# Kernel optimization log

Measured on AMD Instinct MI355X. Metric: run time of the kernel, lower is better.

## Reference

```python
import jax, jax.numpy as jnp
import numpy as np

N_SOURCE = 100000
N_TARGET = 4096
DEG = 800                      # edges per target (uniform)
N_EDGES = N_TARGET * DEG       # 3,276,800
SOURCE_DIM = 512
EMBED_DIM = 32
TARGET_DIM = 16


def setup_inputs() -> dict:
    key = jax.random.key(0)
    k1, k2, k3, k4, k5 = jax.random.split(key, 5)
    source_feat = jax.random.normal(k1, (N_SOURCE, SOURCE_DIM), dtype=jnp.float32)
    embed = jax.random.normal(k2, (SOURCE_DIM, EMBED_DIM), dtype=jnp.float32)
    weight = jax.random.normal(k3, (EMBED_DIM, TARGET_DIM), dtype=jnp.float32)
    # edges sorted by target; range_list[i] = [start, end) of target i's edge block
    src = jax.random.randint(k4, (N_EDGES,), 0, N_SOURCE, dtype=jnp.int64)
    tgt = jnp.repeat(jnp.arange(N_TARGET, dtype=jnp.int64), DEG)
    edge_index = jnp.stack([src, tgt], axis=0)
    starts = jnp.arange(N_TARGET, dtype=jnp.int64) * DEG
    range_list = jnp.stack([starts, starts + DEG], axis=1)
    x_norm = jax.random.uniform(k5, (N_SOURCE,), dtype=jnp.float32) + 0.5
    return {"source_feat": source_feat, "embed": embed, "weight": weight,
            "edge_index": edge_index, "range_list": range_list, "x_norm": x_norm}


def reference(source_feat, embed, weight, edge_index, range_list, x_norm):
    # dense embed GEMM + row normalization
    x = jnp.matmul(source_feat, embed)              # [N_SOURCE, EMBED_DIM]
    x = x / x_norm[:, None]
    # hierarchical conv: gather source rows, mean-aggregate per target segment
    tmp = x[edge_index[0]]                           # [N_EDGES, EMBED_DIM]
    agg = jax.ops.segment_sum(tmp, edge_index[1], num_segments=N_TARGET)
    deg = (range_list[:, 1] - range_list[:, 0]).astype(x.dtype)
    out = agg / jnp.maximum(deg, 1.0)[:, None]       # [N_TARGET, EMBED_DIM]
    out = jnp.matmul(out, weight)                    # [N_TARGET, TARGET_DIM]
    return out
```

## Files before the change

### kernel.cpp

```cpp
#include <hip/hip_runtime.h>
#include <hip/hip_bf16.h>

#define N_SOURCE   100000
#define N_TARGET   4096
#define SOURCE_DIM 512
#define EMBED_DIM  32
#define TARGET_DIM 16
#define NTILES     ((N_SOURCE + 15) / 16)

typedef __attribute__((ext_vector_type(8))) short short8;
typedef __attribute__((ext_vector_type(4))) float f32x4;

static __device__ __forceinline__ ushort f2bf(float f) {
    __hip_bfloat16 h = __float2bfloat16(f);
    return *(ushort*)&h;
}

__global__ __launch_bounds__(256)
void k_embed_weight(const float* __restrict__ embed,
                    const float* __restrict__ weight,
                    ushort* __restrict__ Mt) {
    __shared__ float wlds[EMBED_DIM * TARGET_DIM];
    int tid = threadIdx.x;
    for (int i = tid; i < EMBED_DIM * TARGET_DIM; i += 256)
        wlds[i] = weight[i];
    __syncthreads();

    int idx = blockIdx.x * 256 + tid;
    if (idx < SOURCE_DIM * TARGET_DIM) {
        int k = idx >> 4;
        int o = idx & 15;
        float s = 0.f;
        #pragma unroll
        for (int j = 0; j < EMBED_DIM; ++j)
            s += embed[k * EMBED_DIM + j] * wlds[j * TARGET_DIM + o];
        Mt[o * SOURCE_DIM + k] = f2bf(s);
    }
}

__global__ __launch_bounds__(256, 8)
void k_gemm_y(const float*  __restrict__ A,
              const float*  __restrict__ xnorm,
              const ushort* __restrict__ Mt,
              ushort*       __restrict__ y) {
    __shared__ ushort Bl[SOURCE_DIM * TARGET_DIM];
    int tid  = threadIdx.x;
    int wave = tid >> 6;
    int lane = tid & 63;
    int n    = lane & 15;
    int g    = lane >> 4;

    #pragma unroll
    for (int i = 0; i < 4; ++i) {
        int c  = tid + 256 * i;
        int nn = c & 15;
        int kg = c >> 4;
        int kk = kg >> 2;
        int gg = kg & 3;
        *(uint4*)&Bl[c * 8] =
            *(const uint4*)(Mt + nn * SOURCE_DIM + kk * 32 + gg * 8);
    }
    __syncthreads();

    int tile = blockIdx.x * 4 + wave;
    if (tile < NTILES) {
        int row0 = tile * 16;
        const float* Arow = A + (size_t)(row0 + n) * SOURCE_DIM + g * 8;
        const ushort* Bll = Bl + lane * 8;

        f32x4 acc = {0.f, 0.f, 0.f, 0.f};
        #pragma unroll
        for (int kk = 0; kk < 16; ++kk) {
            float4 a0 = *(const float4*)(Arow + kk * 32);
            float4 a1 = *(const float4*)(Arow + kk * 32 + 4);
            short8 bf = *(const short8*)(Bll + kk * 512);
            short8 af;
            af[0] = (short)f2bf(a0.x); af[1] = (short)f2bf(a0.y);
            af[2] = (short)f2bf(a0.z); af[3] = (short)f2bf(a0.w);
            af[4] = (short)f2bf(a1.x); af[5] = (short)f2bf(a1.y);
            af[6] = (short)f2bf(a1.z); af[7] = (short)f2bf(a1.w);
            acc = __builtin_amdgcn_mfma_f32_16x16x32_bf16(af, bf, acc, 0, 0, 0);
        }

        int m0 = g * 4;
        float4 xn = *(const float4*)(xnorm + row0 + m0);
        const float xr[4] = {xn.x, xn.y, xn.z, xn.w};
        #pragma unroll
        for (int r = 0; r < 4; ++r)
            y[(size_t)(row0 + m0 + r) * TARGET_DIM + n] = f2bf(acc[r] / xr[r]);
    }
}

__global__ __launch_bounds__(256)
void k_gather_mean(const ushort* __restrict__ y,
                   const int*    __restrict__ src,
                   const int*    __restrict__ rl,
                   float* __restrict__ out) {
    int t     = blockIdx.x;
    int tid   = threadIdx.x;
    int start = rl[2 * t];
    int end   = rl[2 * t + 1];

    int slot = tid >> 1;
    int sub  = tid & 1;

    float a[8];
    #pragma unroll
    for (int i = 0; i < 8; ++i) a[i] = 0.f;

    for (int base = start + slot * 4; base < end; base += 512) {
        int rem = end - base;
        int id[4];
        if (rem >= 4) {
            int4 q = *(const int4*)(src + base);
            id[0] = q.x; id[1] = q.y; id[2] = q.z; id[3] = q.w;
        } else {
            #pragma unroll
            for (int j = 0; j < 4; ++j) id[j] = (j < rem) ? src[base + j] : 0;
        }
        #pragma unroll
        for (int j = 0; j < 4; ++j) {
            if (j < rem) {
                uint4 v = *(const uint4*)(y + (size_t)id[j] * TARGET_DIM + sub * 8);
                const uint w[4] = {v.x, v.y, v.z, v.w};
                #pragma unroll
                for (int i = 0; i < 4; ++i) {
                    uint lo = w[i] << 16;
                    uint hi = w[i] & 0xffff0000u;
                    a[2 * i]     += *(float*)&lo;
                    a[2 * i + 1] += *(float*)&hi;
                }
            }
        }
    }

    #pragma unroll
    for (int m = 2; m <= 32; m <<= 1) {
        #pragma unroll
        for (int i = 0; i < 8; ++i) a[i] += __shfl_xor(a[i], m);
    }

    __shared__ float red[4][16];
    int wid  = tid >> 6;
    int lane = tid & 63;
    if (lane < 2) {
        #pragma unroll
        for (int i = 0; i < 8; ++i) red[wid][lane * 8 + i] = a[i];
    }
    __syncthreads();

    if (tid < TARGET_DIM) {
        float s = red[0][tid] + red[1][tid] + red[2][tid] + red[3][tid];
        float deg = (float)(end - start);
        deg = deg > 1.f ? deg : 1.f;
        out[t * TARGET_DIM + tid] = s / deg;
    }
}

extern "C" void kernel_launch(void* const* d_in, const int* in_sizes, int n_in,
                              void* d_out, int out_size, void* d_ws, size_t ws_size,
                              hipStream_t stream) {
    const float* source_feat = (const float*)d_in[0];
    const float* embed       = (const float*)d_in[1];
    const float* weight      = (const float*)d_in[2];
    const int*   edge_src    = (const int*)d_in[3];
    const int*   range_list  = (const int*)d_in[4];
    const float* x_norm      = (const float*)d_in[5];

    float*  out = (float*)d_out;
    ushort* Mt  = (ushort*)d_ws;
    ushort* y   = (ushort*)((char*)d_ws + 16384);

    k_embed_weight<<<32, 256, 0, stream>>>(embed, weight, Mt);

    int nblk = (NTILES + 3) / 4;
    k_gemm_y<<<nblk, 256, 0, stream>>>(source_feat, x_norm, Mt, y);

    k_gather_mean<<<N_TARGET, 256, 0, stream>>>(y, edge_src, range_list, out);
}
```

Baseline: 71.39 us.

## Stage A tiles through swizzled LDS with coalesced loads in embed GEMM

The GEMM kernel now loads each wave's 16x512 fp32 A tile with fully coalesced row-contiguous float4 loads, converts it to bf16, and writes it into a per-wave XOR-swizzled LDS buffer. The MFMA loop then reads its A fragments from LDS instead of doing strided global loads. This is meant to fix the poorly coalesced global access pattern of the A operand. In exchange it uses 80KB of dynamic shared memory per block, which drops occupancy to about two blocks per CU, and adds a block-wide barrier before compute.

```diff
diff --git a/kernel.cpp b/kernel.cpp
--- a/kernel.cpp
+++ b/kernel.cpp
@@ -38,17 +38,17 @@
     }
 }
 
-__global__ __launch_bounds__(256, 8)
+__global__ __launch_bounds__(256, 2)
 void k_gemm_y(const float*  __restrict__ A,
               const float*  __restrict__ xnorm,
               const ushort* __restrict__ Mt,
               ushort*       __restrict__ y) {
-    __shared__ ushort Bl[SOURCE_DIM * TARGET_DIM];
+    extern __shared__ ushort smem[];
+    ushort* Bl  = smem;
     int tid  = threadIdx.x;
     int wave = tid >> 6;
     int lane = tid & 63;
-    int n    = lane & 15;
-    int g    = lane >> 4;
+    ushort* AlW = smem + 8192 + wave * 8192;
 
     #pragma unroll
     for (int i = 0; i < 4; ++i) {
@@ -60,34 +60,51 @@
         *(uint4*)&Bl[c * 8] =
             *(const uint4*)(Mt + nn * SOURCE_DIM + kk * 32 + gg * 8);
     }
+
+    int tile  = blockIdx.x * 4 + wave;
+    int tilec = tile < NTILES ? tile : NTILES - 1;
+    int row0  = tilec * 16;
+
+    int laneConst = ((lane >> 3) << 10) | (((lane >> 1) & 3) << 8) | ((lane & 1) << 3);
+    int xl        = ((laneConst >> 8) & 7);
+
+    #pragma unroll
+    for (int j = 0; j < 32; ++j) {
+        int r = j >> 1, h = j & 1;
+        f32x4 v = *(const f32x4*)(A + (size_t)(row0 + r) * SOURCE_DIM
+                                    + h * 256 + lane * 4);
+        uint d0 = (uint)f2bf(v[0]) | ((uint)f2bf(v[1]) << 16);
+        uint d1 = (uint)f2bf(v[2]) | ((uint)f2bf(v[3]) << 16);
+        int phys = (h << 13) + (laneConst & ~0xF8) + (laneConst & 0x700)
+                 + (laneConst & 0x7C00)
+                 ;
+        phys = laneConst + (h << 13) + ((r ^ xl) << 4);
+        *(uint2*)((char*)AlW + phys) = make_uint2(d0, d1);
+    }
+
     __syncthreads();
 
-    int tile = blockIdx.x * 4 + wave;
     if (tile < NTILES) {
-        int row0 = tile * 16;
-        const float* Arow = A + (size_t)(row0 + n) * SOURCE_DIM + g * 8;
+        int n = lane & 15;
+        int g = lane >> 4;
         const ushort* Bll = Bl + lane * 8;
 
         f32x4 acc = {0.f, 0.f, 0.f, 0.f};
         #pragma unroll
         for (int kk = 0; kk < 16; ++kk) {
-            float4 a0 = *(const float4*)(Arow + kk * 32);
-            float4 a1 = *(const float4*)(Arow + kk * 32 + 4);
-            short8 bf = *(const short8*)(Bll + kk * 512);
-            short8 af;
-            af[0] = (short)f2bf(a0.x); af[1] = (short)f2bf(a0.y);
-            af[2] = (short)f2bf(a0.z); af[3] = (short)f2bf(a0.w);
-            af[4] = (short)f2bf(a1.x); af[5] = (short)f2bf(a1.y);
-            af[6] = (short)f2bf(a1.z); af[7] = (short)f2bf(a1.w);
+            int xr = (4 * kk + (lane >> 4)) & 7;
+            const short8 af = *(const short8*)
+                ((char*)AlW + kk * 1024 + ((lane ^ xr) << 4));
+            const short8 bf = *(const short8*)(Bll + kk * 512);
             acc = __builtin_amdgcn_mfma_f32_16x16x32_bf16(af, bf, acc, 0, 0, 0);
         }
 
         int m0 = g * 4;
         float4 xn = *(const float4*)(xnorm + row0 + m0);
-        const float xr[4] = {xn.x, xn.y, xn.z, xn.w};
+        const float xr4[4] = {xn.x, xn.y, xn.z, xn.w};
         #pragma unroll
         for (int r = 0; r < 4; ++r)
-            y[(size_t)(row0 + m0 + r) * TARGET_DIM + n] = f2bf(acc[r] / xr[r]);
+            y[(size_t)(row0 + m0 + r) * TARGET_DIM + n] = f2bf(acc[r] / xr4[r]);
     }
 }
 
@@ -112,8 +129,8 @@
         int rem = end - base;
         int id[4];
         if (rem >= 4) {
-            int4 q = *(const int4*)(src + base);
-            id[0] = q.x; id[1] = q.y; id[2] = q.z; id[3] = q.w;
+            int4 qd = *(const int4*)(src + base);
+            id[0] = qd.x; id[1] = qd.y; id[2] = qd.z; id[3] = qd.w;
         } else {
             #pragma unroll
             for (int j = 0; j < 4; ++j) id[j] = (j < rem) ? src[base + j] : 0;
@@ -126,9 +143,9 @@
                 #pragma unroll
                 for (int i = 0; i < 4; ++i) {
                     uint lo = w[i] << 16;
-                    uint hi = w[i] & 0xffff0000u;
+                    uint hiw = w[i] & 0xffff0000u;
                     a[2 * i]     += *(float*)&lo;
-                    a[2 * i + 1] += *(float*)&hi;
+                    a[2 * i + 1] += *(float*)&hiw;
                 }
             }
         }
@@ -174,7 +191,7 @@
     k_embed_weight<<<32, 256, 0, stream>>>(embed, weight, Mt);
 
     int nblk = (NTILES + 3) / 4;
-    k_gemm_y<<<nblk, 256, 0, stream>>>(source_feat, x_norm, Mt, y);
+    k_gemm_y<<<nblk, 256, 81920, stream>>>(source_feat, x_norm, Mt, y);
 
     k_gather_mean<<<N_TARGET, 256, 0, stream>>>(y, edge_src, range_list, out);
 }
```

Measured after the change: 61.50 us. -13.9%, faster.
